# Optimization experiments

Hardware: AMD Instinct MI355X
Metric: run time of the kernel (lower is better)

Reference implementation:

```python
import jax, jax.numpy as jnp
import numpy as np

TOP_K = 8


def setup_inputs() -> dict:
    key = jax.random.key(0)
    ks = jax.random.split(key, 6)
    B, S, D, F, E = 2, 1024, 1024, 512, 64
    x = jax.random.normal(ks[0], (B, S, D), dtype=jnp.float32)
    # keras 'random_normal' initializer (stddev=0.05) for centroids
    centroids = jax.random.normal(ks[1], (E, D), dtype=jnp.float32) * 0.05
    expert_biases = jnp.zeros((E,), dtype=jnp.float32)
    # glorot-ish scaling for dense kernels
    Ws_up = jax.random.normal(ks[2], (D, F), dtype=jnp.float32) / np.sqrt(D)
    Ws_down = jax.random.normal(ks[3], (F, D), dtype=jnp.float32) / np.sqrt(F)
    W_up = jax.random.normal(ks[4], (E, D, F), dtype=jnp.float32) / np.sqrt(D)
    W_down = jax.random.normal(ks[5], (E, F, D), dtype=jnp.float32) / np.sqrt(F)
    return {"x": x, "centroids": centroids, "expert_biases": expert_biases,
            "Ws_up": Ws_up, "Ws_down": Ws_down, "W_up": W_up, "W_down": W_down}


def reference(x, centroids, expert_biases, Ws_up, Ws_down, W_up, W_down):
    B, S, D = x.shape
    E = centroids.shape[0]
    T = B * S
    xf = x.reshape(T, D)  # flatten tokens

    # shared expert (num_shared_experts = 1), swish activation, no bias
    shared = jax.nn.silu(xf @ Ws_up) @ Ws_down  # [T, D]

    # affinity routing: top-k on bias-adjusted scores, weights from raw scores
    aff = xf @ centroids.T                        # [T, E]
    biased = aff + expert_biases
    _, idx = jax.lax.top_k(biased, TOP_K)         # [T, K] int32
    sel = jnp.take_along_axis(aff, idx, axis=1)   # gather unbiased scores
    w = jax.nn.sigmoid(sel)
    w = w / (jnp.sum(w, axis=-1, keepdims=True) + 1e-8)  # [T, K]

    # dense combine weights [T, E] (zero where expert not selected)
    cw = jnp.zeros((T, E), dtype=x.dtype).at[jnp.arange(T)[:, None], idx].add(w)

    # routed experts: dense dispatch (equivalent math to masked per-expert FFN)
    h = jax.nn.silu(jnp.einsum('td,edf->etf', xf, W_up))   # [E, T, F]
    y = jnp.einsum('etf,efd->etd', h, W_down)              # [E, T, D]
    routed = jnp.einsum('etd,te->td', y, cw)               # weighted combine

    return (shared + routed).reshape(B, S, D)
```

## Files before the change

### kernel.cpp

```cpp
#include <hip/hip_runtime.h>
#include <math.h>

typedef _Float16 f16;
typedef _Float16 f16x4 __attribute__((ext_vector_type(4)));
typedef _Float16 f16x8 __attribute__((ext_vector_type(8)));
typedef float f32x4 __attribute__((ext_vector_type(4)));

#define T_TOK 2048
#define DDIM  1024
#define FDIM  512
#define NEXP  64
#define TOPK  8
#define NPAIR (T_TOK * TOPK)
#define MAXTILES 192

static constexpr size_t OFF_XH    = 0;
static constexpr size_t OFF_WSUPT = OFF_XH    + (size_t)T_TOK * DDIM * 2;
static constexpr size_t OFF_WSDNT = OFF_WSUPT + (size_t)FDIM * DDIM * 2;
static constexpr size_t OFF_WUPT  = OFF_WSDNT + (size_t)DDIM * FDIM * 2;
static constexpr size_t OFF_WDNT  = OFF_WUPT  + (size_t)NEXP * FDIM * DDIM * 2;
static constexpr size_t OFF_SHH   = OFF_WDNT  + (size_t)NEXP * DDIM * FDIM * 2;
static constexpr size_t OFF_HP    = OFF_SHH   + (size_t)T_TOK * FDIM * 2;
static constexpr size_t OFF_IDX   = OFF_HP    + (size_t)NPAIR * FDIM * 2;
static constexpr size_t OFF_WB    = OFF_IDX   + (size_t)NPAIR * 4;
static constexpr size_t OFF_CNT   = OFF_WB    + (size_t)NPAIR * 4;
static constexpr size_t OFF_OFFS  = OFF_CNT   + 256;
static constexpr size_t OFF_FILL  = OFF_OFFS  + 512;
static constexpr size_t OFF_NT    = OFF_FILL  + 256;
static constexpr size_t OFF_TOK   = OFF_NT    + 256;
static constexpr size_t OFF_PW    = OFF_TOK   + (size_t)NPAIR * 4;
static constexpr size_t OFF_DESC  = OFF_PW    + (size_t)NPAIR * 4;

__device__ __forceinline__ void async_ld16(void* lds, const void* g) {
  __builtin_amdgcn_global_load_lds(
      (const __attribute__((address_space(1))) void*)g,
      (__attribute__((address_space(3))) void*)lds, 16, 0, 0);
}

__global__ void zero_cnt_kernel(int* cnt) {
  if (threadIdx.x < NEXP) cnt[threadIdx.x] = 0;
}

__global__ __launch_bounds__(256)
void transpose_f32_f16_kernel(const float* __restrict__ src0,
                              f16* __restrict__ dst0, int R, int C) {
  __shared__ float tile[64][65];
  const float* src = src0 + (size_t)blockIdx.z * R * C;
  f16* dst = dst0 + (size_t)blockIdx.z * R * C;
  int r0 = blockIdx.y * 64, c0 = blockIdx.x * 64;
  int t = threadIdx.x;
#pragma unroll
  for (int p = 0; p < 4; ++p) {
    int q = t + p * 256;
    int r = q >> 4, c4 = (q & 15) * 4;
    float4 v = *(const float4*)(src + (size_t)(r0 + r) * C + c0 + c4);
    tile[r][c4 + 0] = v.x; tile[r][c4 + 1] = v.y;
    tile[r][c4 + 2] = v.z; tile[r][c4 + 3] = v.w;
  }
  __syncthreads();
#pragma unroll
  for (int p = 0; p < 4; ++p) {
    int q = t + p * 256;
    int rr = q >> 4, cc4 = (q & 15) * 4;
    f16x4 h = { (f16)tile[cc4 + 0][rr], (f16)tile[cc4 + 1][rr],
                (f16)tile[cc4 + 2][rr], (f16)tile[cc4 + 3][rr] };
    *(f16x4*)(dst + (size_t)(c0 + rr) * R + r0 + cc4) = h;
  }
}

__global__ __launch_bounds__(256)
void routing_kernel(const float* __restrict__ x, const float* __restrict__ cent,
                    const float* __restrict__ bias, int* __restrict__ idxbuf,
                    float* __restrict__ wbuf, int* __restrict__ cnt,
                    f16* __restrict__ xh) {
  __shared__ float xs[4][DDIM];
  int t0 = blockIdx.x * 4;
  int tid = threadIdx.x;
#pragma unroll
  for (int p = 0; p < 4; ++p) {
    int q = tid + p * 256;
    int sub = q >> 8, d4 = (q & 255) * 4;
    *(float4*)&xs[sub][d4] = *(const float4*)(x + (size_t)(t0 + sub) * DDIM + d4);
  }
  __syncthreads();
#pragma unroll
  for (int p = 0; p < 4; ++p) {
    int q = tid + p * 256;
    int sub = q >> 8, d4 = (q & 255) * 4;
    f16x4 h = { (f16)xs[sub][d4], (f16)xs[sub][d4 + 1],
                (f16)xs[sub][d4 + 2], (f16)xs[sub][d4 + 3] };
    *(f16x4*)(xh + (size_t)(t0 + sub) * DDIM + d4) = h;
  }
  int lane = tid & 63;
  int sub = tid >> 6;
  int token = t0 + sub;
  const float* c = cent + (size_t)lane * DDIM;
  float aff = 0.f;
  for (int d = 0; d < DDIM; d += 4) {
    float4 cv = *(const float4*)(c + d);
    aff += cv.x * xs[sub][d] + cv.y * xs[sub][d + 1] +
           cv.z * xs[sub][d + 2] + cv.w * xs[sub][d + 3];
  }
  float sc = aff + bias[lane];
  bool picked = false;
  int selidx = 0;
  for (int p = 0; p < TOPK; ++p) {
    float v = picked ? -3.0e38f : sc;
    int ix = lane;
#pragma unroll
    for (int off = 32; off; off >>= 1) {
      float ov = __shfl_xor(v, off);
      int oi = __shfl_xor(ix, off);
      if (ov > v || (ov == v && oi < ix)) { v = ov; ix = oi; }
    }
    if (lane == ix) picked = true;
    if (lane == p) selidx = ix;
  }
  float rawa = __shfl(aff, selidx);
  float s = 1.f / (1.f + expf(-rawa));
  float sum = s;
  sum += __shfl_xor(sum, 1); sum += __shfl_xor(sum, 2); sum += __shfl_xor(sum, 4);
  float wg = s / (sum + 1e-8f);
  if (lane < TOPK) {
    idxbuf[token * TOPK + lane] = selidx;
    wbuf[token * TOPK + lane] = wg;
    atomicAdd(&cnt[selidx], 1);
  }
}

__global__ void scan_desc_kernel(const int* __restrict__ cnt, int* __restrict__ offs,
                                 int* __restrict__ fill, int4* __restrict__ desc,
                                 int* __restrict__ ntiles) {
  if (threadIdx.x < NEXP) fill[threadIdx.x] = 0;
  if (threadIdx.x == 0) {
    int acc = 0, nt = 0;
    for (int e = 0; e < NEXP; ++e) {
      offs[e] = acc;
      int c = cnt[e];
      for (int r = 0; r < c; r += 128)
        desc[nt++] = make_int4(e, acc + r, min(128, c - r), 0);
      acc += c;
    }
    offs[NEXP] = acc;
    *ntiles = nt;
  }
}

__global__ void scatter_kernel(const int* __restrict__ idxbuf, const float* __restrict__ wbuf,
                               const int* __restrict__ offs, int* __restrict__ fill,
                               int* __restrict__ tokb, float* __restrict__ pwb) {
  int gid = blockIdx.x * 256 + threadIdx.x;
  int t = gid >> 3;
  int e = idxbuf[gid];
  int pos = offs[e] + atomicAdd(&fill[e], 1);
  tokb[pos] = t;
  pwb[pos] = wbuf[gid];
}

template <int MODE, bool GATHER_A>
__global__ __launch_bounds__(256)
void gemm_kernel(const f16* __restrict__ A, const f16* __restrict__ Bmat, const int K,
                 const int4* __restrict__ desc, const int* __restrict__ ntiles,
                 const int* __restrict__ tok, const float* __restrict__ pw,
                 void* __restrict__ Out, const int ldo, const long estride) {
  int bx = blockIdx.x, by = blockIdx.y;
  int e = 0, row0, nrows;
  if (desc) {
    if (bx >= *ntiles) return;
    int4 dsc = desc[bx];
    e = dsc.x; row0 = dsc.y; nrows = dsc.z;
  } else {
    row0 = bx * 128; nrows = 128;
  }
  const int n0 = by * 128;
  const f16* Bp = Bmat + (long)e * estride + (long)n0 * K;

  __shared__ f16 As[128 * 32];
  __shared__ f16 Bs[128 * 32];

  const int tid = threadIdx.x;
  const int rA0 = tid >> 2, rA1 = (tid + 256) >> 2;
  const int kq0 = (tid & 3) * 8;
  const int lr0 = min(rA0, nrows - 1), lr1 = min(rA1, nrows - 1);
  long tg0, tg1;
  if (GATHER_A) { tg0 = tok[row0 + lr0]; tg1 = tok[row0 + lr1]; }
  else          { tg0 = row0 + lr0;      tg1 = row0 + lr1; }
  const f16* a0 = A + tg0 * K + kq0;
  const f16* a1 = A + tg1 * K + kq0;
  const f16* b0 = Bp + (long)rA0 * K + kq0;
  const f16* b1 = Bp + (long)rA1 * K + kq0;

  f32x4 acc[4][4] = {};
  const int lane = tid & 63, w = tid >> 6;
  const int wro = (w >> 1) * 64, wco = (w & 1) * 64;
  const int fr = lane & 15, kg = (lane >> 4) * 8;

  for (int k0 = 0; k0 < K; k0 += 32) {
    async_ld16(As + tid * 8,        a0 + k0);
    async_ld16(As + tid * 8 + 2048, a1 + k0);
    async_ld16(Bs + tid * 8,        b0 + k0);
    async_ld16(Bs + tid * 8 + 2048, b1 + k0);
    __syncthreads();
    f16x8 af[4], bf[4];
#pragma unroll
    for (int i = 0; i < 4; ++i)
      af[i] = *(const f16x8*)(As + (wro + i * 16 + fr) * 32 + kg);
#pragma unroll
    for (int j = 0; j < 4; ++j)
      bf[j] = *(const f16x8*)(Bs + (wco + j * 16 + fr) * 32 + kg);
#pragma unroll
    for (int i = 0; i < 4; ++i)
#pragma unroll
      for (int j = 0; j < 4; ++j)
        acc[i][j] = __builtin_amdgcn_mfma_f32_16x16x32_f16(af[i], bf[j], acc[i][j], 0, 0, 0);
    __syncthreads();
  }

#pragma unroll
  for (int i = 0; i < 4; ++i) {
    const int mb = wro + i * 16 + (lane >> 4) * 4;
#pragma unroll
    for (int r = 0; r < 4; ++r) {
      const int m = mb + r;
      if (m >= nrows) continue;
      const long gr = row0 + m;
      float wv = 0.f; long orow = 0;
      if (MODE == 2) { wv = pw[gr]; orow = tok[gr]; }
#pragma unroll
      for (int j = 0; j < 4; ++j) {
        const int col = n0 + wco + j * 16 + fr;
        float v = acc[i][j][r];
        if (MODE == 0) {
          float sv = v / (1.f + expf(-v));
          ((f16*)Out)[gr * ldo + col] = (f16)sv;
        } else if (MODE == 1) {
          ((float*)Out)[gr * ldo + col] = v;
        } else {
          atomicAdd((float*)Out + orow * (long)ldo + col, v * wv);
        }
      }
    }
  }
}

extern "C" void kernel_launch(void* const* d_in, const int* in_sizes, int n_in,
                              void* d_out, int out_size, void* d_ws, size_t ws_size,
                              hipStream_t stream) {
  const float* x    = (const float*)d_in[0];
  const float* cent = (const float*)d_in[1];
  const float* bias = (const float*)d_in[2];
  const float* Wsup = (const float*)d_in[3];
  const float* Wsdn = (const float*)d_in[4];
  const float* Wup  = (const float*)d_in[5];
  const float* Wdn  = (const float*)d_in[6];

  char* ws = (char*)d_ws;
  f16*   xh    = (f16*)(ws + OFF_XH);
  f16*   WsupT = (f16*)(ws + OFF_WSUPT);
  f16*   WsdnT = (f16*)(ws + OFF_WSDNT);
  f16*   WupT  = (f16*)(ws + OFF_WUPT);
  f16*   WdnT  = (f16*)(ws + OFF_WDNT);
  f16*   shh   = (f16*)(ws + OFF_SHH);
  f16*   hp    = (f16*)(ws + OFF_HP);
  int*   idx   = (int*)(ws + OFF_IDX);
  float* wb    = (float*)(ws + OFF_WB);
  int*   cnt   = (int*)(ws + OFF_CNT);
  int*   offs  = (int*)(ws + OFF_OFFS);
  int*   fill  = (int*)(ws + OFF_FILL);
  int*   nt    = (int*)(ws + OFF_NT);
  int*   tokb  = (int*)(ws + OFF_TOK);
  float* pwb   = (float*)(ws + OFF_PW);
  int4*  desc  = (int4*)(ws + OFF_DESC);
  float* out   = (float*)d_out;

  zero_cnt_kernel<<<1, 64, 0, stream>>>(cnt);
  routing_kernel<<<T_TOK / 4, 256, 0, stream>>>(x, cent, bias, idx, wb, cnt, xh);
  transpose_f32_f16_kernel<<<dim3(FDIM / 64, DDIM / 64, 1), 256, 0, stream>>>(Wsup, WsupT, DDIM, FDIM);
  transpose_f32_f16_kernel<<<dim3(DDIM / 64, FDIM / 64, 1), 256, 0, stream>>>(Wsdn, WsdnT, FDIM, DDIM);
  transpose_f32_f16_kernel<<<dim3(FDIM / 64, DDIM / 64, NEXP), 256, 0, stream>>>(Wup, WupT, DDIM, FDIM);
  transpose_f32_f16_kernel<<<dim3(DDIM / 64, FDIM / 64, NEXP), 256, 0, stream>>>(Wdn, WdnT, FDIM, DDIM);
  scan_desc_kernel<<<1, 64, 0, stream>>>(cnt, offs, fill, desc, nt);
  scatter_kernel<<<NPAIR / 256, 256, 0, stream>>>(idx, wb, offs, fill, tokb, pwb);

  gemm_kernel<0, false><<<dim3(T_TOK / 128, FDIM / 128), 256, 0, stream>>>(
      xh, WsupT, DDIM, nullptr, nullptr, nullptr, nullptr, shh, FDIM, 0);
  gemm_kernel<0, true><<<dim3(MAXTILES, FDIM / 128), 256, 0, stream>>>(
      xh, WupT, DDIM, desc, nt, tokb, nullptr, hp, FDIM, (long)FDIM * DDIM);
  gemm_kernel<1, false><<<dim3(T_TOK / 128, DDIM / 128), 256, 0, stream>>>(
      shh, WsdnT, FDIM, nullptr, nullptr, nullptr, nullptr, out, DDIM, 0);
  gemm_kernel<2, false><<<dim3(MAXTILES, DDIM / 128), 256, 0, stream>>>(
      hp, WdnT, FDIM, desc, nt, tokb, pwb, out, DDIM, (long)DDIM * FDIM);
}
```

Measured before the change: 620.1 us.

## Drop weight transpose pre-pass, convert fp32 weights in GEMM B-load, merge shared expert

Removes the separate transpose/convert kernels that rewrote all expert weights to fp16 each call. The GEMM now reads fp32 weights directly in their native layout, converts them in registers and packs them into padded LDS. The shared-expert up-projection is folded into the routed up-GEMM as an extra expert with identity tokens. Routing is split into a tiled affinity GEMM and a separate top-k kernel. This saves a full read-write pass over the roughly 256MB of expert weights, but the GEMM must now read fp32 B (twice the bytes per tile) through non-async loads, with conversion work inside the main loop.

```diff
diff --git a/kernel.cpp b/kernel.cpp
--- a/kernel.cpp
+++ b/kernel.cpp
@@ -2,6 +2,7 @@
 #include <math.h>
 
 typedef _Float16 f16;
+typedef _Float16 f16x2 __attribute__((ext_vector_type(2)));
 typedef _Float16 f16x4 __attribute__((ext_vector_type(4)));
 typedef _Float16 f16x8 __attribute__((ext_vector_type(8)));
 typedef float f32x4 __attribute__((ext_vector_type(4)));
@@ -12,24 +13,22 @@
 #define NEXP  64
 #define TOPK  8
 #define NPAIR (T_TOK * TOPK)
+#define NSHT  (T_TOK / 128)
 #define MAXTILES 192
-
-static constexpr size_t OFF_XH    = 0;
-static constexpr size_t OFF_WSUPT = OFF_XH    + (size_t)T_TOK * DDIM * 2;
-static constexpr size_t OFF_WSDNT = OFF_WSUPT + (size_t)FDIM * DDIM * 2;
-static constexpr size_t OFF_WUPT  = OFF_WSDNT + (size_t)DDIM * FDIM * 2;
-static constexpr size_t OFF_WDNT  = OFF_WUPT  + (size_t)NEXP * FDIM * DDIM * 2;
-static constexpr size_t OFF_SHH   = OFF_WDNT  + (size_t)NEXP * DDIM * FDIM * 2;
-static constexpr size_t OFF_HP    = OFF_SHH   + (size_t)T_TOK * FDIM * 2;
-static constexpr size_t OFF_IDX   = OFF_HP    + (size_t)NPAIR * FDIM * 2;
-static constexpr size_t OFF_WB    = OFF_IDX   + (size_t)NPAIR * 4;
-static constexpr size_t OFF_CNT   = OFF_WB    + (size_t)NPAIR * 4;
-static constexpr size_t OFF_OFFS  = OFF_CNT   + 256;
-static constexpr size_t OFF_FILL  = OFF_OFFS  + 512;
-static constexpr size_t OFF_NT    = OFF_FILL  + 256;
-static constexpr size_t OFF_TOK   = OFF_NT    + 256;
-static constexpr size_t OFF_PW    = OFF_TOK   + (size_t)NPAIR * 4;
-static constexpr size_t OFF_DESC  = OFF_PW    + (size_t)NPAIR * 4;
+#define HPROWS (NPAIR + T_TOK)
+
+static constexpr size_t OFF_XH   = 0;
+static constexpr size_t OFF_AFF  = OFF_XH  + (size_t)T_TOK * DDIM * 2;
+static constexpr size_t OFF_HPA  = OFF_AFF + (size_t)T_TOK * NEXP * 4;
+static constexpr size_t OFF_IDX  = OFF_HPA + (size_t)HPROWS * FDIM * 2;
+static constexpr size_t OFF_WB   = OFF_IDX + (size_t)NPAIR * 4;
+static constexpr size_t OFF_CNT  = OFF_WB  + (size_t)NPAIR * 4;
+static constexpr size_t OFF_OFFS = OFF_CNT + 256;
+static constexpr size_t OFF_FILL = OFF_OFFS + 512;
+static constexpr size_t OFF_NTS  = OFF_FILL + 256;
+static constexpr size_t OFF_TOK  = OFF_NTS + 256;
+static constexpr size_t OFF_PW   = OFF_TOK + (size_t)HPROWS * 4;
+static constexpr size_t OFF_DESC = OFF_PW  + (size_t)HPROWS * 4;
 
 __device__ __forceinline__ void async_ld16(void* lds, const void* g) {
   __builtin_amdgcn_global_load_lds(
@@ -42,66 +41,64 @@
 }
 
 __global__ __launch_bounds__(256)
-void transpose_f32_f16_kernel(const float* __restrict__ src0,
-                              f16* __restrict__ dst0, int R, int C) {
-  __shared__ float tile[64][65];
-  const float* src = src0 + (size_t)blockIdx.z * R * C;
-  f16* dst = dst0 + (size_t)blockIdx.z * R * C;
-  int r0 = blockIdx.y * 64, c0 = blockIdx.x * 64;
-  int t = threadIdx.x;
-#pragma unroll
-  for (int p = 0; p < 4; ++p) {
-    int q = t + p * 256;
-    int r = q >> 4, c4 = (q & 15) * 4;
-    float4 v = *(const float4*)(src + (size_t)(r0 + r) * C + c0 + c4);
-    tile[r][c4 + 0] = v.x; tile[r][c4 + 1] = v.y;
-    tile[r][c4 + 2] = v.z; tile[r][c4 + 3] = v.w;
-  }
-  __syncthreads();
-#pragma unroll
-  for (int p = 0; p < 4; ++p) {
-    int q = t + p * 256;
-    int rr = q >> 4, cc4 = (q & 15) * 4;
-    f16x4 h = { (f16)tile[cc4 + 0][rr], (f16)tile[cc4 + 1][rr],
-                (f16)tile[cc4 + 2][rr], (f16)tile[cc4 + 3][rr] };
-    *(f16x4*)(dst + (size_t)(c0 + rr) * R + r0 + cc4) = h;
-  }
+void aff_kernel(const float* __restrict__ x, const float* __restrict__ cent,
+                float* __restrict__ aff, f16* __restrict__ xh) {
+  __shared__ __align__(16) float xs[32 * 132];
+  __shared__ __align__(16) float cs[64 * 128];
+  const int tid = threadIdx.x;
+  const int t0 = blockIdx.x * 32;
+  const int tg = tid >> 4;
+  const int eg = tid & 15;
+  float acc0[4] = {0.f, 0.f, 0.f, 0.f};
+  float acc1[4] = {0.f, 0.f, 0.f, 0.f};
+  for (int kc = 0; kc < DDIM / 128; ++kc) {
+    const int kbase = kc * 128;
+#pragma unroll
+    for (int p = 0; p < 4; ++p) {
+      int u = tid + p * 256;
+      int row = u >> 5, kk4 = u & 31;
+      float4 v = *(const float4*)(x + (size_t)(t0 + row) * DDIM + kbase + kk4 * 4);
+      *(float4*)&xs[row * 132 + kk4 * 4] = v;
+      f16x4 h = {(f16)v.x, (f16)v.y, (f16)v.z, (f16)v.w};
+      *(f16x4*)(xh + (size_t)(t0 + row) * DDIM + kbase + kk4 * 4) = h;
+    }
+#pragma unroll
+    for (int p = 0; p < 8; ++p) {
+      int u = tid + p * 256;
+      int e = u >> 5, kk4 = u & 31;
+      float4 v = *(const float4*)(cent + (size_t)e * DDIM + kbase + kk4 * 4);
+      *(float4*)&cs[e * 128 + ((kk4 ^ ((e >> 2) & 7)) << 2)] = v;
+    }
+    __syncthreads();
+#pragma unroll 4
+    for (int kk4 = 0; kk4 < 32; ++kk4) {
+      float4 xa0 = *(const float4*)&xs[tg * 132 + kk4 * 4];
+      float4 xa1 = *(const float4*)&xs[(tg + 16) * 132 + kk4 * 4];
+#pragma unroll
+      for (int j = 0; j < 4; ++j) {
+        int e = eg * 4 + j;
+        float4 cb = *(const float4*)&cs[e * 128 + ((kk4 ^ (eg & 7)) << 2)];
+        acc0[j] += xa0.x * cb.x + xa0.y * cb.y + xa0.z * cb.z + xa0.w * cb.w;
+        acc1[j] += xa1.x * cb.x + xa1.y * cb.y + xa1.z * cb.z + xa1.w * cb.w;
+      }
+    }
+    __syncthreads();
+  }
+  float4 o0 = {acc0[0], acc0[1], acc0[2], acc0[3]};
+  float4 o1 = {acc1[0], acc1[1], acc1[2], acc1[3]};
+  *(float4*)(aff + (size_t)(t0 + tg) * NEXP + eg * 4) = o0;
+  *(float4*)(aff + (size_t)(t0 + tg + 16) * NEXP + eg * 4) = o1;
 }
 
 __global__ __launch_bounds__(256)
-void routing_kernel(const float* __restrict__ x, const float* __restrict__ cent,
-                    const float* __restrict__ bias, int* __restrict__ idxbuf,
-                    float* __restrict__ wbuf, int* __restrict__ cnt,
-                    f16* __restrict__ xh) {
-  __shared__ float xs[4][DDIM];
-  int t0 = blockIdx.x * 4;
+void topk_kernel(const float* __restrict__ aff, const float* __restrict__ bias,
+                 int* __restrict__ idxbuf, float* __restrict__ wbuf,
+                 int* __restrict__ cnt) {
   int tid = threadIdx.x;
-#pragma unroll
-  for (int p = 0; p < 4; ++p) {
-    int q = tid + p * 256;
-    int sub = q >> 8, d4 = (q & 255) * 4;
-    *(float4*)&xs[sub][d4] = *(const float4*)(x + (size_t)(t0 + sub) * DDIM + d4);
-  }
-  __syncthreads();
-#pragma unroll
-  for (int p = 0; p < 4; ++p) {
-    int q = tid + p * 256;
-    int sub = q >> 8, d4 = (q & 255) * 4;
-    f16x4 h = { (f16)xs[sub][d4], (f16)xs[sub][d4 + 1],
-                (f16)xs[sub][d4 + 2], (f16)xs[sub][d4 + 3] };
-    *(f16x4*)(xh + (size_t)(t0 + sub) * DDIM + d4) = h;
-  }
-  int lane = tid & 63;
-  int sub = tid >> 6;
-  int token = t0 + sub;
-  const float* c = cent + (size_t)lane * DDIM;
-  float aff = 0.f;
-  for (int d = 0; d < DDIM; d += 4) {
-    float4 cv = *(const float4*)(c + d);
-    aff += cv.x * xs[sub][d] + cv.y * xs[sub][d + 1] +
-           cv.z * xs[sub][d + 2] + cv.w * xs[sub][d + 3];
-  }
-  float sc = aff + bias[lane];
+  int lane = tid & 63, sub = tid >> 6;
+  int token = blockIdx.x * 4 + sub;
+  float a = aff[(size_t)token * NEXP + lane];
+  float sc = a + bias[lane];
   bool picked = false;
   int selidx = 0;
   for (int p = 0; p < TOPK; ++p) {
@@ -116,7 +113,7 @@
     if (lane == ix) picked = true;
     if (lane == p) selidx = ix;
   }
-  float rawa = __shfl(aff, selidx);
+  float rawa = __shfl(a, selidx);
   float s = 1.f / (1.f + expf(-rawa));
   float sum = s;
   sum += __shfl_xor(sum, 1); sum += __shfl_xor(sum, 2); sum += __shfl_xor(sum, 4);
@@ -130,7 +127,7 @@
 
 __global__ void scan_desc_kernel(const int* __restrict__ cnt, int* __restrict__ offs,
                                  int* __restrict__ fill, int4* __restrict__ desc,
-                                 int* __restrict__ ntiles) {
+                                 int* __restrict__ nts) {
   if (threadIdx.x < NEXP) fill[threadIdx.x] = 0;
   if (threadIdx.x == 0) {
     int acc = 0, nt = 0;
@@ -142,7 +139,10 @@
       acc += c;
     }
     offs[NEXP] = acc;
-    *ntiles = nt;
+    nts[1] = nt;
+    for (int i = 0; i < NSHT; ++i)
+      desc[nt++] = make_int4(NEXP, NPAIR + i * 128, 128, 0);
+    nts[0] = nt;
   }
 }
 
@@ -150,16 +150,22 @@
                                const int* __restrict__ offs, int* __restrict__ fill,
                                int* __restrict__ tokb, float* __restrict__ pwb) {
   int gid = blockIdx.x * 256 + threadIdx.x;
-  int t = gid >> 3;
-  int e = idxbuf[gid];
-  int pos = offs[e] + atomicAdd(&fill[e], 1);
-  tokb[pos] = t;
-  pwb[pos] = wbuf[gid];
+  if (gid < NPAIR) {
+    int t = gid >> 3;
+    int e = idxbuf[gid];
+    int pos = offs[e] + atomicAdd(&fill[e], 1);
+    tokb[pos] = t;
+    pwb[pos] = wbuf[gid];
+  } else {
+    tokb[gid] = gid - NPAIR;
+    pwb[gid] = 1.0f;
+  }
 }
 
 template <int MODE, bool GATHER_A>
 __global__ __launch_bounds__(256)
-void gemm_kernel(const f16* __restrict__ A, const f16* __restrict__ Bmat, const int K,
+void gemm_kernel(const f16* __restrict__ A, const float* __restrict__ Bmat,
+                 const float* __restrict__ B2, const int K, const int ldb,
                  const int4* __restrict__ desc, const int* __restrict__ ntiles,
                  const int* __restrict__ tok, const float* __restrict__ pw,
                  void* __restrict__ Out, const int ldo, const long estride) {
@@ -173,10 +179,10 @@
     row0 = bx * 128; nrows = 128;
   }
   const int n0 = by * 128;
-  const f16* Bp = Bmat + (long)e * estride + (long)n0 * K;
-
-  __shared__ f16 As[128 * 32];
-  __shared__ f16 Bs[128 * 32];
+  const float* Bp = (e == NEXP) ? (B2 + n0) : (Bmat + (long)e * estride + n0);
+
+  __shared__ __align__(16) f16 As[128 * 32];
+  __shared__ __align__(16) f16 Bs[128 * 40];
 
   const int tid = threadIdx.x;
   const int rA0 = tid >> 2, rA1 = (tid + 256) >> 2;
@@ -187,8 +193,9 @@
   else          { tg0 = row0 + lr0;      tg1 = row0 + lr1; }
   const f16* a0 = A + tg0 * K + kq0;
   const f16* a1 = A + tg1 * K + kq0;
-  const f16* b0 = Bp + (long)rA0 * K + kq0;
-  const f16* b1 = Bp + (long)rA1 * K + kq0;
+  const int ukp = tid & 15, un4 = tid >> 4;
+  const float* bg = Bp + (size_t)(2 * ukp) * ldb + un4 * 4;
+  f16x2* bsw = (f16x2*)Bs;
 
   f32x4 acc[4][4] = {};
   const int lane = tid & 63, w = tid >> 6;
@@ -198,8 +205,20 @@
   for (int k0 = 0; k0 < K; k0 += 32) {
     async_ld16(As + tid * 8,        a0 + k0);
     async_ld16(As + tid * 8 + 2048, a1 + k0);
-    async_ld16(Bs + tid * 8,        b0 + k0);
-    async_ld16(Bs + tid * 8 + 2048, b1 + k0);
+    const float* bgk = bg + (size_t)k0 * ldb;
+    float4 v0 = *(const float4*)bgk;
+    float4 v1 = *(const float4*)(bgk + ldb);
+    float4 v2 = *(const float4*)(bgk + 64);
+    float4 v3 = *(const float4*)(bgk + ldb + 64);
+#pragma unroll
+    for (int i = 0; i < 4; ++i) {
+      float a0i = (i == 0) ? v0.x : (i == 1) ? v0.y : (i == 2) ? v0.z : v0.w;
+      float b0i = (i == 0) ? v1.x : (i == 1) ? v1.y : (i == 2) ? v1.z : v1.w;
+      float a1i = (i == 0) ? v2.x : (i == 1) ? v2.y : (i == 2) ? v2.z : v2.w;
+      float b1i = (i == 0) ? v3.x : (i == 1) ? v3.y : (i == 2) ? v3.z : v3.w;
+      bsw[(un4 * 4 + i) * 20 + ukp]        = f16x2{(f16)a0i, (f16)b0i};
+      bsw[((un4 + 16) * 4 + i) * 20 + ukp] = f16x2{(f16)a1i, (f16)b1i};
+    }
     __syncthreads();
     f16x8 af[4], bf[4];
 #pragma unroll
@@ -207,7 +226,7 @@
       af[i] = *(const f16x8*)(As + (wro + i * 16 + fr) * 32 + kg);
 #pragma unroll
     for (int j = 0; j < 4; ++j)
-      bf[j] = *(const f16x8*)(Bs + (wco + j * 16 + fr) * 32 + kg);
+      bf[j] = *(const f16x8*)(Bs + (wco + j * 16 + fr) * 40 + kg);
 #pragma unroll
     for (int i = 0; i < 4; ++i)
 #pragma unroll
@@ -255,39 +274,33 @@
   const float* Wdn  = (const float*)d_in[6];
 
   char* ws = (char*)d_ws;
-  f16*   xh    = (f16*)(ws + OFF_XH);
-  f16*   WsupT = (f16*)(ws + OFF_WSUPT);
-  f16*   WsdnT = (f16*)(ws + OFF_WSDNT);
-  f16*   WupT  = (f16*)(ws + OFF_WUPT);
-  f16*   WdnT  = (f16*)(ws + OFF_WDNT);
-  f16*   shh   = (f16*)(ws + OFF_SHH);
-  f16*   hp    = (f16*)(ws + OFF_HP);
-  int*   idx   = (int*)(ws + OFF_IDX);
-  float* wb    = (float*)(ws + OFF_WB);
-  int*   cnt   = (int*)(ws + OFF_CNT);
-  int*   offs  = (int*)(ws + OFF_OFFS);
-  int*   fill  = (int*)(ws + OFF_FILL);
-  int*   nt    = (int*)(ws + OFF_NT);
-  int*   tokb  = (int*)(ws + OFF_TOK);
-  float* pwb   = (float*)(ws + OFF_PW);
-  int4*  desc  = (int4*)(ws + OFF_DESC);
-  float* out   = (float*)d_out;
+  f16*   xh   = (f16*)(ws + OFF_XH);
+  float* aff  = (float*)(ws + OFF_AFF);
+  f16*   hpa  = (f16*)(ws + OFF_HPA);
+  int*   idx  = (int*)(ws + OFF_IDX);
+  float* wb   = (float*)(ws + OFF_WB);
+  int*   cnt  = (int*)(ws + OFF_CNT);
+  int*   offs = (int*)(ws + OFF_OFFS);
+  int*   fill = (int*)(ws + OFF_FILL);
+  int*   nts  = (int*)(ws + OFF_NTS);
+  int*   tokb = (int*)(ws + OFF_TOK);
+  float* pwb  = (float*)(ws + OFF_PW);
+  int4*  desc = (int4*)(ws + OFF_DESC);
+  float* out  = (float*)d_out;
 
   zero_cnt_kernel<<<1, 64, 0, stream>>>(cnt);
-  routing_kernel<<<T_TOK / 4, 256, 0, stream>>>(x, cent, bias, idx, wb, cnt, xh);
-  transpose_f32_f16_kernel<<<dim3(FDIM / 64, DDIM / 64, 1), 256, 0, stream>>>(Wsup, WsupT, DDIM, FDIM);
-  transpose_f32_f16_kernel<<<dim3(DDIM / 64, FDIM / 64, 1), 256, 0, stream>>>(Wsdn, WsdnT, FDIM, DDIM);
-  transpose_f32_f16_kernel<<<dim3(FDIM / 64, DDIM / 64, NEXP), 256, 0, stream>>>(Wup, WupT, DDIM, FDIM);
-  transpose_f32_f16_kernel<<<dim3(DDIM / 64, FDIM / 64, NEXP), 256, 0, stream>>>(Wdn, WdnT, FDIM, DDIM);
-  scan_desc_kernel<<<1, 64, 0, stream>>>(cnt, offs, fill, desc, nt);
-  scatter_kernel<<<NPAIR / 256, 256, 0, stream>>>(idx, wb, offs, fill, tokb, pwb);
-
-  gemm_kernel<0, false><<<dim3(T_TOK / 128, FDIM / 128), 256, 0, stream>>>(
-      xh, WsupT, DDIM, nullptr, nullptr, nullptr, nullptr, shh, FDIM, 0);
-  gemm_kernel<0, true><<<dim3(MAXTILES, FDIM / 128), 256, 0, stream>>>(
-      xh, WupT, DDIM, desc, nt, tokb, nullptr, hp, FDIM, (long)FDIM * DDIM);
+  aff_kernel<<<T_TOK / 32, 256, 0, stream>>>(x, cent, aff, xh);
+  topk_kernel<<<T_TOK / 4, 256, 0, stream>>>(aff, bias, idx, wb, cnt);
+  scan_desc_kernel<<<1, 64, 0, stream>>>(cnt, offs, fill, desc, nts);
+  scatter_kernel<<<HPROWS / 256, 256, 0, stream>>>(idx, wb, offs, fill, tokb, pwb);
+
+  gemm_kernel<0, true><<<dim3(MAXTILES + NSHT, FDIM / 128), 256, 0, stream>>>(
+      xh, Wup, Wsup, DDIM, FDIM, desc, &nts[0], tokb, nullptr, hpa, FDIM,
+      (long)DDIM * FDIM);
   gemm_kernel<1, false><<<dim3(T_TOK / 128, DDIM / 128), 256, 0, stream>>>(
-      shh, WsdnT, FDIM, nullptr, nullptr, nullptr, nullptr, out, DDIM, 0);
+      hpa + (size_t)NPAIR * FDIM, Wsdn, nullptr, FDIM, DDIM,
+      nullptr, nullptr, nullptr, nullptr, out, DDIM, 0);
   gemm_kernel<2, false><<<dim3(MAXTILES, DDIM / 128), 256, 0, stream>>>(
-      hp, WdnT, FDIM, desc, nt, tokb, pwb, out, DDIM, (long)DDIM * FDIM);
-}
+      hpa, Wdn, nullptr, FDIM, DDIM, desc, &nts[1], tokb, pwb, out, DDIM,
+      (long)FDIM * DDIM);
+}
```

New measurement: 571.0 us. 7.9% less time.
